# Kernel optimization log

Hardware: AMD Instinct MI355X
Metric: run time of the kernel (lower is better)

The kernel has to match this reference:

```python
import jax, jax.numpy as jnp
import numpy as np

H = 4      # num_heads
F = 64     # node_in_feats
FE = 16    # edge_in_feats
N = 4096   # num_nodes
E = 65536  # num_edges (avg degree 16)


def setup_inputs() -> dict:
    key = jax.random.key(0)
    ks = jax.random.split(key, 6)
    return {
        "node_inputs": jax.random.normal(ks[0], (N, F), jnp.float32),
        "edge_inputs": jax.random.normal(ks[1], (E, FE), jnp.float32),
        "src": jax.random.randint(ks[2], (E,), 0, N, jnp.int32),
        "dst": jax.random.randint(ks[3], (E,), 0, N, jnp.int32),
        "Wn": jax.random.normal(ks[4], (F, F * H), jnp.float32) / np.sqrt(F).astype(np.float32),
        "bn": jnp.zeros((F * H,), jnp.float32),
        "We": jax.random.normal(ks[5], (FE, H), jnp.float32) / np.sqrt(FE).astype(np.float32),
        "be": jnp.zeros((H,), jnp.float32),
    }


def reference(node_inputs, edge_inputs, src, dst, Wn, bn, We, be):
    # node linear projection: [N, H*F] then torch .view(H, -1, F) == row-major reshape
    node_proj = (node_inputs @ Wn + bn).reshape(H, N, F)
    # edge linear projection: [E, H] then torch .view(H, -1, 1) == row-major reshape
    edge_proj = (edge_inputs @ We + be).reshape(H, E)
    # self-attention: scale by sqrt(edge_in_feats), softmax over dim=1 (all edges per head)
    attn = jax.nn.softmax(edge_proj / np.float32(np.sqrt(FE)), axis=1)  # [H, E]
    # dense attention projection: projection[h, src[e], dst[e]] = attn[h, e]
    proj = jnp.zeros((H, N, N), jnp.float32).at[:, src, dst].set(attn)  # [H, N, N]
    # message passing ('sum' aggregation): proj @ node_proj -> [H, N, F]
    msg = jnp.einsum('hsd,hdf->hsf', proj, node_proj)
    # head pooling 'mean' over head dim (-3)
    return msg.mean(axis=0)  # [N, F]
```

## Files before the change

### kernel.cpp

```cpp
#include <hip/hip_runtime.h>

#define TBL_BITS 18
#define TBL_SIZE (1u << TBL_BITS)
#define TBL_MASK (TBL_SIZE - 1u)

#define GBLK 1024
#define BLK  256


struct Args {
    const float* X;  const float* Xe;
    const int* src;  const int* dst;
    const float* Wn; const float* bn;
    const float* We; const float* be;
    float* out;
    float* nproj;
    float* ep;
    float* partials;
    unsigned long long* tbl;
};

__device__ __forceinline__ unsigned hash_key(unsigned key) {
    return (key * 2654435761u) >> (32 - TBL_BITS);
}

__global__ __launch_bounds__(BLK, 4) void k_a(Args A) {
    const int tid = blockIdx.x * BLK + threadIdx.x;
    {
        const float4 z = make_float4(0.f, 0.f, 0.f, 0.f);
        if (tid < 65536)       ((float4*)A.out)[tid] = z;
        else if (tid < 196608) ((float4*)A.tbl)[tid - 65536] = z;
    }
    if (tid < 131072) {
        const int c = tid & 255;
        const int g = tid >> 8;
        const float b = A.bn[c];
        float acc[8];
#pragma unroll
        for (int r = 0; r < 8; ++r) acc[r] = b;
        const float* Wc = A.Wn + c;
#pragma unroll 8
        for (int k = 0; k < 64; ++k) {
            const float w = Wc[k * 256];
#pragma unroll
            for (int r = 0; r < 8; ++r)
                acc[r] = fmaf(A.X[(g + 512 * r) * 64 + k], w, acc[r]);
        }
#pragma unroll
        for (int r = 0; r < 8; ++r)
            A.nproj[(g + 512 * r) * 256 + c] = acc[r];
    }
    if (tid < 65536) {
        const float4* xi = (const float4*)(A.Xe + (size_t)tid * 16);
        float x[16];
        float4 v;
        v = xi[0]; x[0]=v.x;  x[1]=v.y;  x[2]=v.z;  x[3]=v.w;
        v = xi[1]; x[4]=v.x;  x[5]=v.y;  x[6]=v.z;  x[7]=v.w;
        v = xi[2]; x[8]=v.x;  x[9]=v.y;  x[10]=v.z; x[11]=v.w;
        v = xi[3]; x[12]=v.x; x[13]=v.y; x[14]=v.z; x[15]=v.w;
        float a0 = A.be[0], a1 = A.be[1], a2 = A.be[2], a3 = A.be[3];
#pragma unroll
        for (int k = 0; k < 16; ++k) {
            a0 = fmaf(x[k], A.We[k * 4 + 0], a0);
            a1 = fmaf(x[k], A.We[k * 4 + 1], a1);
            a2 = fmaf(x[k], A.We[k * 4 + 2], a2);
            a3 = fmaf(x[k], A.We[k * 4 + 3], a3);
        }
        const float e0 = expf(a0 * 0.25f), e1 = expf(a1 * 0.25f);
        const float e2 = expf(a2 * 0.25f), e3 = expf(a3 * 0.25f);
        ((float4*)A.ep)[tid] = make_float4(e0, e1, e2, e3);
        float s = e0 + e1 + e2 + e3;
#pragma unroll
        for (int off = 32; off > 0; off >>= 1) s += __shfl_xor(s, off);
        if ((tid & 63) == 0) A.partials[tid >> 6] = s;
    }
}

__global__ __launch_bounds__(BLK, 4) void k_b(Args A) {
    __shared__ float4 red[256];
    __shared__ float s_stats[4];
    {
        const int t = threadIdx.x;
        red[t] = make_float4(A.partials[t], A.partials[256 + t],
                             A.partials[512 + t], A.partials[768 + t]);
        __syncthreads();
        for (int s = 128; s > 0; s >>= 1) {
            if (t < s) {
                red[t].x += red[t + s].x; red[t].y += red[t + s].y;
                red[t].z += red[t + s].z; red[t].w += red[t + s].w;
            }
            __syncthreads();
        }
        if (t == 0) {
            s_stats[0] = 0.25f / red[0].x;
            s_stats[1] = 0.25f / red[0].y;
            s_stats[2] = 0.25f / red[0].z;
            s_stats[3] = 0.25f / red[0].w;
        }
        __syncthreads();
    }
    const float r0 = s_stats[0], r1 = s_stats[1];
    const float r2 = s_stats[2], r3 = s_stats[3];

    const int tid  = blockIdx.x * BLK + threadIdx.x;
    const int w    = tid >> 6;
    const int lane = tid & 63;

#pragma unroll
    for (int i = 0; i < 8; i += 4) {
        const int ebase = w * 8 + i;
        int action = 0;
        int sub_e  = -1;
        if (lane < 4) {
            const int e = ebase + lane;
            const unsigned key = ((unsigned)A.src[e] << 12) | (unsigned)A.dst[e];
            const unsigned long long tag  = (unsigned long long)(key + 1u);
            const unsigned long long pack = (tag << 24) | (unsigned long long)e;
            unsigned idx = hash_key(key);
            while (true) {
                unsigned long long cur = A.tbl[idx];
                if (cur == 0ull) {
                    unsigned long long old = atomicCAS(&A.tbl[idx], 0ull, pack);
                    if (old == 0ull) { action = 1; break; }
                    cur = old;
                }
                if ((cur >> 24) == tag) {
                    const unsigned long long old = atomicMax(&A.tbl[idx], pack);
                    if (old < pack) {
                        action = 1;
                        sub_e = (int)(old & 0xFFFFFFull);
                    }
                    break;
                }
                idx = (idx + 1u) & TBL_MASK;
            }
        }
#pragma unroll
        for (int j = 0; j < 4; ++j) {
            const int act = __shfl(action, j);
            if (!act) continue;
            const int e  = ebase + j;
            const int sj = A.src[e];
            const int dj = A.dst[e];
            const int se = __shfl(sub_e, j);
            float c0 = A.ep[e];
            float c1 = A.ep[65536 + e];
            float c2 = A.ep[131072 + e];
            float c3 = A.ep[196608 + e];
            if (se >= 0) {
                c0 -= A.ep[se];
                c1 -= A.ep[65536 + se];
                c2 -= A.ep[131072 + se];
                c3 -= A.ep[196608 + se];
            }
            const int base = dj * 64 + lane;
            float v = c0 * r0 * A.nproj[base];
            v = fmaf(c1 * r1, A.nproj[base + 262144], v);
            v = fmaf(c2 * r2, A.nproj[base + 524288], v);
            v = fmaf(c3 * r3, A.nproj[base + 786432], v);
            unsafeAtomicAdd(&A.out[sj * 64 + lane], v);
        }
    }
}

extern "C" void kernel_launch(void* const* d_in, const int* in_sizes, int n_in,
                              void* d_out, int out_size, void* d_ws, size_t ws_size,
                              hipStream_t stream) {
    Args A;
    A.X   = (const float*)d_in[0];
    A.Xe  = (const float*)d_in[1];
    A.src = (const int*)d_in[2];
    A.dst = (const int*)d_in[3];
    A.Wn  = (const float*)d_in[4];
    A.bn  = (const float*)d_in[5];
    A.We  = (const float*)d_in[6];
    A.be  = (const float*)d_in[7];
    A.out = (float*)d_out;
    char* ws   = (char*)d_ws;
    A.nproj    = (float*)ws;
    A.ep       = (float*)(ws + 4u * 1024u * 1024u);
    A.partials = (float*)(ws + 5u * 1024u * 1024u);
    A.tbl      = (unsigned long long*)(ws + 6u * 1024u * 1024u);

    k_a<<<GBLK, BLK, 0, stream>>>(A);
    k_b<<<2048, BLK, 0, stream>>>(A);
}
```

Before: 46.42 us.

## Shrink hash table, split k_a work ranges, batch 8-edge hash probes in k_b

The dedup hash table is halved, which cuts zero-init traffic, and k_a now gives edge projection its own thread range so fewer blocks are launched. In k_b all 8 edges per wave are probed in one pass, with src/dst values shuffled from the probing lanes instead of reloaded. The probes are also issued before the softmax-sum reduction, which is now a single float4 load plus wave shuffles instead of a shared-memory tree. A smaller table raises load factor and probe lengths, and two table lookups are no longer serialised.

New measurement: 51.16 us. 1.1x slower.

```diff
diff --git a/kernel.cpp b/kernel.cpp
--- a/kernel.cpp
+++ b/kernel.cpp
@@ -1,10 +1,10 @@
 #include <hip/hip_runtime.h>
 
-#define TBL_BITS 18
+#define TBL_BITS 17
 #define TBL_SIZE (1u << TBL_BITS)
 #define TBL_MASK (TBL_SIZE - 1u)
 
-#define GBLK 1024
+#define GBLK 768
 #define BLK  256
 
 
@@ -29,7 +29,7 @@
     {
         const float4 z = make_float4(0.f, 0.f, 0.f, 0.f);
         if (tid < 65536)       ((float4*)A.out)[tid] = z;
-        else if (tid < 196608) ((float4*)A.tbl)[tid - 65536] = z;
+        else if (tid < 131072) ((float4*)A.tbl)[tid - 65536] = z;
     }
     if (tid < 131072) {
         const int c = tid & 255;
@@ -49,9 +49,9 @@
 #pragma unroll
         for (int r = 0; r < 8; ++r)
             A.nproj[(g + 512 * r) * 256 + c] = acc[r];
-    }
-    if (tid < 65536) {
-        const float4* xi = (const float4*)(A.Xe + (size_t)tid * 16);
+    } else {
+        const int e = tid - 131072;
+        const float4* xi = (const float4*)(A.Xe + (size_t)e * 16);
         float x[16];
         float4 v;
         v = xi[0]; x[0]=v.x;  x[1]=v.y;  x[2]=v.z;  x[3]=v.w;
@@ -68,98 +68,84 @@
         }
         const float e0 = expf(a0 * 0.25f), e1 = expf(a1 * 0.25f);
         const float e2 = expf(a2 * 0.25f), e3 = expf(a3 * 0.25f);
-        ((float4*)A.ep)[tid] = make_float4(e0, e1, e2, e3);
+        ((float4*)A.ep)[e] = make_float4(e0, e1, e2, e3);
         float s = e0 + e1 + e2 + e3;
 #pragma unroll
         for (int off = 32; off > 0; off >>= 1) s += __shfl_xor(s, off);
-        if ((tid & 63) == 0) A.partials[tid >> 6] = s;
+        if ((e & 63) == 0) A.partials[e >> 6] = s;
     }
 }
 
 __global__ __launch_bounds__(BLK, 4) void k_b(Args A) {
-    __shared__ float4 red[256];
+    const int tid  = blockIdx.x * BLK + threadIdx.x;
+    const int w    = tid >> 6;
+    const int lane = tid & 63;
+
+    int action = 0, sub_e = -1, sv = 0, dv = 0;
+    if (lane < 8) {
+        const int e = w * 8 + lane;
+        sv = A.src[e];
+        dv = A.dst[e];
+        const unsigned key = ((unsigned)sv << 12) | (unsigned)dv;
+        const unsigned long long tag  = (unsigned long long)(key + 1u);
+        const unsigned long long pack = (tag << 24) | (unsigned long long)e;
+        unsigned idx = hash_key(key);
+        while (true) {
+            unsigned long long cur = A.tbl[idx];
+            if (cur == 0ull) {
+                unsigned long long old = atomicCAS(&A.tbl[idx], 0ull, pack);
+                if (old == 0ull) { action = 1; break; }
+                cur = old;
+            }
+            if ((cur >> 24) == tag) {
+                const unsigned long long old = atomicMax(&A.tbl[idx], pack);
+                if (old < pack) {
+                    action = 1;
+                    sub_e = (int)(old & 0xFFFFFFull);
+                }
+                break;
+            }
+            idx = (idx + 1u) & TBL_MASK;
+        }
+    }
+
     __shared__ float s_stats[4];
     {
         const int t = threadIdx.x;
-        red[t] = make_float4(A.partials[t], A.partials[256 + t],
-                             A.partials[512 + t], A.partials[768 + t]);
-        __syncthreads();
-        for (int s = 128; s > 0; s >>= 1) {
-            if (t < s) {
-                red[t].x += red[t + s].x; red[t].y += red[t + s].y;
-                red[t].z += red[t + s].z; red[t].w += red[t + s].w;
-            }
-            __syncthreads();
-        }
-        if (t == 0) {
-            s_stats[0] = 0.25f / red[0].x;
-            s_stats[1] = 0.25f / red[0].y;
-            s_stats[2] = 0.25f / red[0].z;
-            s_stats[3] = 0.25f / red[0].w;
-        }
+        const float4 p = ((const float4*)A.partials)[t];
+        float s = p.x + p.y + p.z + p.w;
+#pragma unroll
+        for (int off = 32; off > 0; off >>= 1) s += __shfl_xor(s, off);
+        if ((t & 63) == 0) s_stats[t >> 6] = 0.25f / s;
         __syncthreads();
     }
     const float r0 = s_stats[0], r1 = s_stats[1];
     const float r2 = s_stats[2], r3 = s_stats[3];
 
-    const int tid  = blockIdx.x * BLK + threadIdx.x;
-    const int w    = tid >> 6;
-    const int lane = tid & 63;
-
 #pragma unroll
-    for (int i = 0; i < 8; i += 4) {
-        const int ebase = w * 8 + i;
-        int action = 0;
-        int sub_e  = -1;
-        if (lane < 4) {
-            const int e = ebase + lane;
-            const unsigned key = ((unsigned)A.src[e] << 12) | (unsigned)A.dst[e];
-            const unsigned long long tag  = (unsigned long long)(key + 1u);
-            const unsigned long long pack = (tag << 24) | (unsigned long long)e;
-            unsigned idx = hash_key(key);
-            while (true) {
-                unsigned long long cur = A.tbl[idx];
-                if (cur == 0ull) {
-                    unsigned long long old = atomicCAS(&A.tbl[idx], 0ull, pack);
-                    if (old == 0ull) { action = 1; break; }
-                    cur = old;
-                }
-                if ((cur >> 24) == tag) {
-                    const unsigned long long old = atomicMax(&A.tbl[idx], pack);
-                    if (old < pack) {
-                        action = 1;
-                        sub_e = (int)(old & 0xFFFFFFull);
-                    }
-                    break;
-                }
-                idx = (idx + 1u) & TBL_MASK;
-            }
+    for (int j = 0; j < 8; ++j) {
+        const int act = __shfl(action, j);
+        if (!act) continue;
+        const int e  = w * 8 + j;
+        const int sj = __shfl(sv, j);
+        const int dj = __shfl(dv, j);
+        const int se = __shfl(sub_e, j);
+        float c0 = A.ep[e];
+        float c1 = A.ep[65536 + e];
+        float c2 = A.ep[131072 + e];
+        float c3 = A.ep[196608 + e];
+        if (se >= 0) {
+            c0 -= A.ep[se];
+            c1 -= A.ep[65536 + se];
+            c2 -= A.ep[131072 + se];
+            c3 -= A.ep[196608 + se];
         }
-#pragma unroll
-        for (int j = 0; j < 4; ++j) {
-            const int act = __shfl(action, j);
-            if (!act) continue;
-            const int e  = ebase + j;
-            const int sj = A.src[e];
-            const int dj = A.dst[e];
-            const int se = __shfl(sub_e, j);
-            float c0 = A.ep[e];
-            float c1 = A.ep[65536 + e];
-            float c2 = A.ep[131072 + e];
-            float c3 = A.ep[196608 + e];
-            if (se >= 0) {
-                c0 -= A.ep[se];
-                c1 -= A.ep[65536 + se];
-                c2 -= A.ep[131072 + se];
-                c3 -= A.ep[196608 + se];
-            }
-            const int base = dj * 64 + lane;
-            float v = c0 * r0 * A.nproj[base];
-            v = fmaf(c1 * r1, A.nproj[base + 262144], v);
-            v = fmaf(c2 * r2, A.nproj[base + 524288], v);
-            v = fmaf(c3 * r3, A.nproj[base + 786432], v);
-            unsafeAtomicAdd(&A.out[sj * 64 + lane], v);
-        }
+        const int base = dj * 64 + lane;
+        float v = c0 * r0 * A.nproj[base];
+        v = fmaf(c1 * r1, A.nproj[base + 262144], v);
+        v = fmaf(c2 * r2, A.nproj[base + 524288], v);
+        v = fmaf(c3 * r3, A.nproj[base + 786432], v);
+        unsafeAtomicAdd(&A.out[sj * 64 + lane], v);
     }
 }
 
```
